# Kernel optimization log

Measured on AMD Instinct MI355X. Metric: run time of the kernel, lower is better.

## Reference

```python
import jax, jax.numpy as jnp
import numpy as np

B, Q, H, W, C = 2, 8192, 64, 64, 64
C9 = C * 9
EPS = 1e-6


def _mlp(x, params):
    # gelu MLP, no activation on last layer (matches repo mlp)
    for Wm, b in params[:-1]:
        x = jax.nn.gelu(x @ Wm + b)
    Wl, bl = params[-1]
    return x @ Wl + bl


def _make_coord(h, w):
    # pixel-center coords in (-1,1); channel 0 = row dim, channel 1 = col dim
    hs = -1.0 + (2.0 * jnp.arange(h, dtype=jnp.float32) + 1.0) / h
    ws = -1.0 + (2.0 * jnp.arange(w, dtype=jnp.float32) + 1.0) / w
    return jnp.stack(jnp.meshgrid(hs, ws, indexing='ij'), axis=0)  # (2,h,w)


def _nearest_gather(feat, coord):
    # F.grid_sample(mode='nearest', align_corners=False) on a (B,1,q,2) grid.
    # feat (B,C,H,W); coord (B,q,2) with [...,0] indexing H, [...,1] indexing W
    h, w = feat.shape[-2], feat.shape[-1]
    ih = jnp.clip(jnp.round((coord[..., 0] + 1.0) * h / 2.0 - 0.5), 0, h - 1).astype(jnp.int32)
    iw = jnp.clip(jnp.round((coord[..., 1] + 1.0) * w / 2.0 - 0.5), 0, w - 1).astype(jnp.int32)
    return jax.vmap(lambda f, a, b: f[:, a, b].T)(feat, ih, iw)  # (B,q,C)


def _unfold3(feat):
    # F.unfold(feat, 3, padding=1).view(B, C*9, H, W): channel-major, kernel row-major
    b, c, h, w = feat.shape
    p = jnp.pad(feat, ((0, 0), (0, 0), (1, 1), (1, 1)))
    patches = jnp.stack([p[:, :, i:i + h, j:j + w] for i in range(3) for j in range(3)], axis=2)
    return patches.reshape(b, c * 9, h, w)


def _forward(inp, coord, scale, enc_w, enc_b, iw0, ib0, iw1, ib1, iw2, ib2,
             sw0, sb0, sw1, sb1, ww0, wb0, ww1, wb1):
    # encoder (stand-in conv3x3, 3 -> C feature channels)
    feat = jax.lax.conv_general_dilated(inp, enc_w, (1, 1), 'SAME',
                                        dimension_numbers=('NCHW', 'OIHW', 'NCHW'))
    feat = feat + enc_b[None, :, None, None]
    feat = _unfold3(feat)  # (B, C*9, H, W)
    bsz, cf, h, w = feat.shape
    fcoord = jnp.broadcast_to(_make_coord(h, w)[None], (bsz, 2, h, w))
    dims = jnp.array([h, w], dtype=feat.dtype)

    tx = (h - 1) / (1.0 - scale[:, 0, 0])  # (B,)
    ty = (w - 1) / (1.0 - scale[:, 0, 1])
    rx, ry = 1.0 / tx, 1.0 / ty
    scale_tok = scale * dims  # (B,q,2)

    imnet_p = [(iw0, ib0), (iw1, ib1), (iw2, ib2)]
    score_p = [(sw0, sb0), (sw1, sb1)]
    weight_p = [(ww0, wb0), (ww1, wb1)]

    preds = []
    for vx in (-1, 1):
        for vy in (-1, 1):
            shift = jnp.stack([vx * rx + EPS, vy * ry + EPS], axis=-1)[:, None, :]  # (B,1,2)
            c = jnp.clip(coord + shift, -1.0 + 1e-6, 1.0 - 1e-6)
            value = _nearest_gather(feat, c)      # (B,q,C*9)
            coord_k = _nearest_gather(fcoord, c)  # (B,q,2)
            rel = (coord - coord_k) * dims        # (B,q,2)
            score = _mlp(rel, score_p)            # (B,q,1) -> broadcast over 3
            mlp_in = jnp.concatenate([rel, scale_tok], axis=-1)  # (B,q,4)
            wmat = _mlp(mlp_in, imnet_p).reshape(bsz, -1, cf, 3)  # (B,q,C*9,3)
            preds.append(jnp.einsum('bqc,bqck->bqk', value, wmat) + score)
    stacked = jnp.stack(preds, axis=-1)  # (B,q,3,4)
    return _mlp(stacked, weight_p)[..., 0]  # (B,q,3)


def setup_inputs() -> dict:
    key = jax.random.key(0)
    ks = jax.random.split(key, 16)
    f32 = jnp.float32

    def wi(k, shape, fan_in):
        return jax.random.normal(k, shape, f32) / np.float32(np.sqrt(fan_in))

    return {
        'inp': jax.random.normal(ks[0], (B, 3, H, W), f32),
        'coord': jax.random.uniform(ks[1], (B, Q, 2), f32, -1.0 + 1e-4, 1.0 - 1e-4),
        'scale': jax.random.uniform(ks[2], (B, Q, 2), f32, 0.01, 0.05),
        'enc_w': wi(ks[3], (C, 3, 3, 3), 27),
        'enc_b': jnp.zeros((C,), f32),
        'iw0': wi(ks[4], (4, 256), 4), 'ib0': jnp.zeros((256,), f32),
        'iw1': wi(ks[5], (256, 256), 256), 'ib1': jnp.zeros((256,), f32),
        'iw2': wi(ks[6], (256, C9 * 3), 256), 'ib2': jnp.zeros((C9 * 3,), f32),
        'sw0': wi(ks[7], (2, 256), 2), 'sb0': jnp.zeros((256,), f32),
        'sw1': wi(ks[8], (256, 1), 256), 'sb1': jnp.zeros((1,), f32),
        'ww0': wi(ks[9], (4, 256), 4), 'wb0': jnp.zeros((256,), f32),
        'ww1': wi(ks[10], (256, 1), 256), 'wb1': jnp.zeros((1,), f32),
    }


def reference(inp, coord, scale, enc_w, enc_b, iw0, ib0, iw1, ib1, iw2, ib2,
              sw0, sb0, sw1, sb1, ww0, wb0, ww1, wb1):
    return _forward(inp, coord, scale, enc_w, enc_b, iw0, ib0, iw1, ib1, iw2, ib2,
                    sw0, sb0, sw1, sb1, ww0, wb0, ww1, wb1)
```

## Files before the change

### kernel.cpp

```cpp
#include <hip/hip_runtime.h>

#define QN 8192
#define CCH 64
#define NROW 65536
#define MR 32
#define NBLK (NROW / MR)
#define H0S 264
#define UW 784
#define SVP 592

typedef _Float16 f16x8 __attribute__((ext_vector_type(8)));
typedef _Float16 f16x4 __attribute__((ext_vector_type(4)));
typedef _Float16 f16x2 __attribute__((ext_vector_type(2)));
typedef float f32x4 __attribute__((ext_vector_type(4)));

#if __has_builtin(__builtin_amdgcn_fdot2)
#define FDOT2(A, B, C) __builtin_amdgcn_fdot2((A), (B), (C), false)
#else
#define FDOT2(A, B, C) fmaf((float)(A)[1], (float)(B)[1], fmaf((float)(A)[0], (float)(B)[0], (C)))
#endif
#define DOT8(H, U, ACC) do {                                                                      \
    ACC = FDOT2(((f16x2){(H)[0], (H)[1]}), ((f16x2){(U)[0], (U)[1]}), ACC);                       \
    ACC = FDOT2(((f16x2){(H)[2], (H)[3]}), ((f16x2){(U)[2], (U)[3]}), ACC);                       \
    ACC = FDOT2(((f16x2){(H)[4], (H)[5]}), ((f16x2){(U)[4], (U)[5]}), ACC);                       \
    ACC = FDOT2(((f16x2){(H)[6], (H)[7]}), ((f16x2){(U)[6], (U)[7]}), ACC);                       \
} while (0)

__device__ __forceinline__ float gelu_f(float x) {
    float x2 = x * x;
    float tt = fmaf(0.044715f, x2, 1.0f);
    float e = __builtin_amdgcn_exp2f(2.3022081597f * x * tt);
    float r = __builtin_amdgcn_rcpf(1.0f + e);
    return x - x * r;
}

__global__ __launch_bounds__(256) void k_pre(const float* __restrict__ inp,
                                             const float* __restrict__ ew,
                                             const float* __restrict__ eb,
                                             const float* __restrict__ coord,
                                             const float* __restrict__ scale,
                                             const float* __restrict__ sw0,
                                             const float* __restrict__ sb0,
                                             const float* __restrict__ sw1,
                                             const float* __restrict__ sb1,
                                             const float* __restrict__ iw1,
                                             const float* __restrict__ iw2,
                                             const float* __restrict__ ib2,
                                             float* __restrict__ featpad,
                                             float4* __restrict__ mlp_in,
                                             int2* __restrict__ ihiw,
                                             float* __restrict__ scoreg,
                                             _Float16* __restrict__ w1tp,
                                             _Float16* __restrict__ w3tp) {
    const int bb = blockIdx.x;
    const int tt0 = threadIdx.x;
    if (bb < 2178) {
        __shared__ float s_ew[1728];
        for (int i = tt0; i < 1728; i += 256) s_ew[i] = ew[i];
        __syncthreads();
        int idx = bb * 256 + tt0;
        const int total = 2 * 66 * 66 * CCH;
        if (idx >= total) return;
        int o = idx & 63; int pix = idx >> 6;
        int xx = pix % 66; int t2 = pix / 66;
        int yy = t2 % 66;  int b = t2 / 66;
        int y = yy - 1, x = xx - 1;
        float acc = 0.0f;
        if (y >= 0 && y < 64 && x >= 0 && x < 64) {
            acc = eb[o];
            for (int i = 0; i < 3; ++i) {
                const float* ip = inp + ((b * 3 + i) * 64) * 64;
                const float* wp = s_ew + (o * 3 + i) * 9;
                #pragma unroll
                for (int ky = 0; ky < 3; ++ky) {
                    int sy = y + ky - 1;
                    if (sy < 0 || sy > 63) continue;
                    #pragma unroll
                    for (int kx = 0; kx < 3; ++kx) {
                        int sx = x + kx - 1;
                        if (sx < 0 || sx > 63) continue;
                        acc += ip[sy * 64 + sx] * wp[ky * 3 + kx];
                    }
                }
            }
        }
        featpad[idx] = acc;
    } else if (bb < 2434) {
        int row = (bb - 2178) * 256 + tt0;
        int v = row & 3;
        int bq = row >> 2;
        int b = bq >> 13;
        float c0 = coord[bq * 2 + 0], c1 = coord[bq * 2 + 1];
        float s0 = scale[bq * 2 + 0], s1 = scale[bq * 2 + 1];
        float s00 = scale[(b * QN) * 2 + 0];
        float s01 = scale[(b * QN) * 2 + 1];
        float rx = (1.0f - s00) / 63.0f;
        float ry = (1.0f - s01) / 63.0f;
        float vx = (v & 2) ? 1.0f : -1.0f;
        float vy = (v & 1) ? 1.0f : -1.0f;
        float cc0 = c0 + vx * rx + 1e-6f;
        float cc1 = c1 + vy * ry + 1e-6f;
        cc0 = fminf(fmaxf(cc0, -1.0f + 1e-6f), 1.0f - 1e-6f);
        cc1 = fminf(fmaxf(cc1, -1.0f + 1e-6f), 1.0f - 1e-6f);
        int ih = (int)rintf((cc0 + 1.0f) * 32.0f - 0.5f);
        int iw = (int)rintf((cc1 + 1.0f) * 32.0f - 0.5f);
        ih = min(max(ih, 0), 63);
        iw = min(max(iw, 0), 63);
        float ck0 = (2.0f * (float)ih + 1.0f) / 64.0f - 1.0f;
        float ck1 = (2.0f * (float)iw + 1.0f) / 64.0f - 1.0f;
        float rel0 = (c0 - ck0) * 64.0f;
        float rel1 = (c1 - ck1) * 64.0f;
        mlp_in[row] = make_float4(rel0, rel1, s0 * 64.0f, s1 * 64.0f);
        ihiw[row] = make_int2(ih, iw);
        float sc = sb1[0];
        #pragma unroll 4
        for (int t2 = 0; t2 < 256; ++t2) {
            float h = gelu_f(fmaf(rel0, sw0[t2], fmaf(rel1, sw0[256 + t2], sb0[t2])));
            sc = fmaf(h, sw1[t2], sc);
        }
        scoreg[row] = sc;
    } else {
        int idx = (bb - 2434) * 256 + tt0;
        if (idx < 451584) {
            int jj = idx & 7, ln = (idx >> 3) & 63;
            int tlkf = idx >> 9;
            int tl = tlkf / 18, kf = tlkf - tl * 18;
            int o = tl * 16 + (ln & 15);
            int v = kf * 32 + (ln >> 4) * 8 + jj;
            int tap = v >> 6, cch = v & 63;
            float val = 0.0f;
            if (o < 768) {
                int j = o & 255, k = o >> 8;
                val = iw2[j * 1728 + (cch * 9 + tap) * 3 + k];
            } else if (o < 771) {
                val = ib2[(cch * 9 + tap) * 3 + (o - 768)];
            }
            w3tp[idx] = (_Float16)val;
        } else {
            int i2 = idx - 451584;
            int j = i2 & 7, ln = (i2 >> 3) & 63, kf = (i2 >> 9) & 7, ct = i2 >> 12;
            int col = ct * 16 + (ln & 15);
            int kk = kf * 32 + (ln >> 4) * 8 + j;
            w1tp[i2] = (_Float16)iw1[kk * 256 + col];
        }
    }
}

__global__ __launch_bounds__(256) void k_u(const float* __restrict__ featpad,
                                           const _Float16* __restrict__ w3tp,
                                           _Float16* __restrict__ u) {
    __shared__ __align__(16) _Float16 s_val[32 * SVP];
    __shared__ int s_dtab[9];
    const int t = threadIdx.x;
    const int wave = t >> 6, lane = t & 63, quad = lane >> 4, l15 = lane & 15;
    if (t < 9) { int dy = t / 3; s_dtab[t] = (dy * 66 + (t - 3 * dy)) * 64; }
    {
        int p = t & 31, half = t >> 5;
        int slot = blockIdx.x * 32 + p;
        int b = slot >> 12, rem = slot & 4095, y = rem >> 6, x = rem & 63;
        int base = ((b * 66 + y) * 66 + x) * 64;
        __syncthreads();
        #pragma unroll
        for (int i = 0; i < 18; ++i) {
            int v0 = half * 72 + i * 4;
            int tap = v0 >> 6, cch = v0 & 63;
            float4 f = *(const float4*)(featpad + base + s_dtab[tap] + cch);
            f16x4 hv = {(_Float16)f.x, (_Float16)f.y, (_Float16)f.z, (_Float16)f.w};
            *(f16x4*)(s_val + p * SVP + v0) = hv;
        }
    }
    __syncthreads();

    const int t0 = (wave == 0) ? 0 : 1 + wave * 12;
    const int nt = (wave == 0) ? 13 : 12;
    #pragma unroll 1
    for (int tt = 0; tt < nt; ++tt) {
        int tl = t0 + tt;
        const _Float16* wp = w3tp + ((size_t)(tl * 18) * 64 + lane) * 8;
        f16x8 bbuf[18];
        #pragma unroll
        for (int kf = 0; kf < 18; ++kf) bbuf[kf] = *(const f16x8*)(wp + (size_t)kf * 512);
        f32x4 ac0 = {0.f, 0.f, 0.f, 0.f}, ac1 = {0.f, 0.f, 0.f, 0.f};
        #pragma unroll
        for (int kf = 0; kf < 18; ++kf) {
            f16x8 a0 = *(const f16x8*)(s_val + l15 * SVP + kf * 32 + quad * 8);
            f16x8 a1 = *(const f16x8*)(s_val + (16 + l15) * SVP + kf * 32 + quad * 8);
            ac0 = __builtin_amdgcn_mfma_f32_16x16x32_f16(a0, bbuf[kf], ac0, 0, 0, 0);
            ac1 = __builtin_amdgcn_mfma_f32_16x16x32_f16(a1, bbuf[kf], ac1, 0, 0, 0);
        }
        size_t pb = (size_t)(blockIdx.x * 32 + quad * 4) * UW + tl * 16 + l15;
        #pragma unroll
        for (int rg = 0; rg < 4; ++rg) u[pb + (size_t)rg * UW] = (_Float16)ac0[rg];
        pb += (size_t)16 * UW;
        #pragma unroll
        for (int rg = 0; rg < 4; ++rg) u[pb + (size_t)rg * UW] = (_Float16)ac1[rg];
    }
}

#define LDX1(B, CT) do { const _Float16* wp_ = w1tp + (size_t)((CT) * 8) * 512 + lane * 8;        \
    _Pragma("unroll") for (int kf_ = 0; kf_ < 4; ++kf_) B[kf_] = *(const f16x8*)(wp_ + kf_ * 512); } while (0)
#define LDY1(B, CT) do { const _Float16* wp_ = w1tp + (size_t)((CT) * 8 + 4) * 512 + lane * 8;    \
    _Pragma("unroll") for (int kf_ = 0; kf_ < 4; ++kf_) B[kf_] = *(const f16x8*)(wp_ + kf_ * 512); } while (0)
#define ZACCB(BV) do { _Pragma("unroll") for (int rt_ = 0; rt_ < 2; ++rt_)                        \
    acc[rt_] = (f32x4){(BV), (BV), (BV), (BV)}; } while (0)
#define MFMAH(B, OFS) do { _Pragma("unroll") for (int kf_ = 0; kf_ < 4; ++kf_)                    \
    { _Pragma("unroll") for (int rt_ = 0; rt_ < 2; ++rt_)                                         \
      acc[rt_] = __builtin_amdgcn_mfma_f32_16x16x32_f16(a[rt_][kf_ + (OFS)], B[kf_], acc[rt_], 0, 0, 0); } } while (0)
#define H1EPI(CT) do { int col_ = (CT) * 16 + l15;                                                \
    _Pragma("unroll") for (int rt_ = 0; rt_ < 2; ++rt_)                                           \
      { _Pragma("unroll") for (int rg_ = 0; rg_ < 4; ++rg_)                                       \
        s_h0[(rt_ * 16 + quad * 4 + rg_) * H0S + col_] = (_Float16)gelu_f(acc[rt_][rg_]); } } while (0)

__global__ __launch_bounds__(256, 3) void k_dot(const float4* __restrict__ mlp_in,
                                                const int2* __restrict__ ihiw,
                                                const float* __restrict__ iw0,
                                                const float* __restrict__ ib0,
                                                const _Float16* __restrict__ w1tp,
                                                const float* __restrict__ ib1,
                                                const _Float16* __restrict__ ubuf,
                                                const float* __restrict__ scoreg,
                                                const float* __restrict__ ww0,
                                                const float* __restrict__ wb0,
                                                const float* __restrict__ ww1,
                                                const float* __restrict__ wb1,
                                                float* __restrict__ out) {
    __shared__ __align__(16) _Float16 s_h0[MR * H0S];
    __shared__ float4 s_min[MR];
    __shared__ int    s_slot[MR];
    __shared__ float  s_pred[MR][3];
    __shared__ float  s_score[MR];
    __shared__ float  s_dred[MR][3][8];
    __shared__ float  s_wred[24][4];

    const int t = threadIdx.x;
    const int wave = t >> 6, lane = t & 63, quad = lane >> 4, l15 = lane & 15;
    const int rowbase = blockIdx.x * MR;

    if (t < MR) {
        int row = rowbase + t;
        s_min[t] = mlp_in[row];
        s_score[t] = scoreg[row];
        int b = row >> 15;
        int2 p = ihiw[row];
        s_slot[t] = (b << 12) + (p.x << 6) + p.y;
    }
    __syncthreads();

    {
        float w0 = iw0[t], w1 = iw0[256 + t], w2 = iw0[512 + t], w3 = iw0[768 + t];
        float bb = ib0[t];
        #pragma unroll 4
        for (int r = 0; r < MR; ++r) {
            float4 m = s_min[r];
            s_h0[r * H0S + t] =
                (_Float16)gelu_f(fmaf(m.x, w0, fmaf(m.y, w1, fmaf(m.z, w2, fmaf(m.w, w3, bb)))));
        }
    }
    __syncthreads();

    const int w4 = wave * 4;
    const float bibA = ib1[(w4 + 0) * 16 + l15];
    const float bibB = ib1[(w4 + 1) * 16 + l15];
    const float bibC = ib1[(w4 + 2) * 16 + l15];
    const float bibD = ib1[(w4 + 3) * 16 + l15];

    f16x8 bX0[4], bX1[4], bY0[4], bY1[4];
    f32x4 acc[2];

    LDX1(bX0, w4);
    LDY1(bY0, w4);
    LDX1(bX1, w4 + 1);

    f16x8 a[2][8];
    #pragma unroll
    for (int rt = 0; rt < 2; ++rt)
        #pragma unroll
        for (int kf = 0; kf < 8; ++kf)
            a[rt][kf] = *(const f16x8*)(s_h0 + (rt * 16 + l15) * H0S + kf * 32 + quad * 8);
    __syncthreads();

    LDY1(bY1, w4 + 1);
    ZACCB(bibA); MFMAH(bX0, 0);
    LDX1(bX0, w4 + 2);
    MFMAH(bY0, 4);
    H1EPI(w4);
    LDY1(bY0, w4 + 2);
    ZACCB(bibB); MFMAH(bX1, 0);
    LDX1(bX1, w4 + 3);
    MFMAH(bY1, 4);
    H1EPI(w4 + 1);
    LDY1(bY1, w4 + 3);
    ZACCB(bibC); MFMAH(bX0, 0);
    MFMAH(bY0, 4);
    H1EPI(w4 + 2);
    ZACCB(bibD); MFMAH(bX1, 0);
    MFMAH(bY1, 4);
    H1EPI(w4 + 3);
    __syncthreads();

    {
        int r = t >> 3, sub = t & 7;
        int j0 = sub * 32;
        const _Float16* hb = s_h0 + r * H0S + j0;
        const _Float16* ub = ubuf + (size_t)s_slot[r] * UW + j0;
        float a0 = 0.f, a1 = 0.f, a2 = 0.f;
        #pragma unroll
        for (int c = 0; c < 4; ++c) {
            f16x8 h8 = *(const f16x8*)(hb + c * 8);
            f16x8 u0 = *(const f16x8*)(ub + c * 8);
            f16x8 u1 = *(const f16x8*)(ub + 256 + c * 8);
            f16x8 u2 = *(const f16x8*)(ub + 512 + c * 8);
            DOT8(h8, u0, a0);
            DOT8(h8, u1, a1);
            DOT8(h8, u2, a2);
        }
        s_dred[r][0][sub] = a0;
        s_dred[r][1][sub] = a1;
        s_dred[r][2][sub] = a2;
    }
    __syncthreads();
    if (t < 96) {
        int r = t / 3, k = t - 3 * r;
        float s = (float)ubuf[(size_t)s_slot[r] * UW + 768 + k];
        #pragma unroll
        for (int q = 0; q < 8; ++q) s += s_dred[r][k][q];
        s_pred[r][k] = s;
    }
    __syncthreads();

    if (t < 96) {
        int o = t >> 2, sub = t & 3;
        int bql = o / 3, k = o - 3 * bql;
        float x0 = s_pred[bql * 4 + 0][k] + s_score[bql * 4 + 0];
        float x1 = s_pred[bql * 4 + 1][k] + s_score[bql * 4 + 1];
        float x2 = s_pred[bql * 4 + 2][k] + s_score[bql * 4 + 2];
        float x3 = s_pred[bql * 4 + 3][k] + s_score[bql * 4 + 3];
        float acc2 = 0.0f;
        int j0 = sub * 64;
        #pragma unroll 4
        for (int j = j0; j < j0 + 64; ++j) {
            float h = gelu_f(fmaf(x0, ww0[j], fmaf(x1, ww0[256 + j],
                          fmaf(x2, ww0[512 + j], fmaf(x3, ww0[768 + j], wb0[j])))));
            acc2 = fmaf(h, ww1[j], acc2);
        }
        s_wred[o][sub] = acc2;
    }
    __syncthreads();
    if (t < 24) {
        int bql = t / 3, k = t - 3 * bql;
        float r2 = s_wred[t][0] + s_wred[t][1] + s_wred[t][2] + s_wred[t][3] + wb1[0];
        out[(blockIdx.x * 8 + bql) * 3 + k] = r2;
    }
}

extern "C" void kernel_launch(void* const* d_in, const int* in_sizes, int n_in,
                              void* d_out, int out_size, void* d_ws, size_t ws_size,
                              hipStream_t stream) {
    const float* inp   = (const float*)d_in[0];
    const float* coord = (const float*)d_in[1];
    const float* scale = (const float*)d_in[2];
    const float* ew    = (const float*)d_in[3];
    const float* eb    = (const float*)d_in[4];
    const float* iw0   = (const float*)d_in[5];
    const float* ib0   = (const float*)d_in[6];
    const float* iw1   = (const float*)d_in[7];
    const float* ib1   = (const float*)d_in[8];
    const float* iw2   = (const float*)d_in[9];
    const float* ib2   = (const float*)d_in[10];
    const float* sw0   = (const float*)d_in[11];
    const float* sb0   = (const float*)d_in[12];
    const float* sw1   = (const float*)d_in[13];
    const float* sb1   = (const float*)d_in[14];
    const float* ww0   = (const float*)d_in[15];
    const float* wb0   = (const float*)d_in[16];
    const float* ww1   = (const float*)d_in[17];
    const float* wb1   = (const float*)d_in[18];
    float* out = (float*)d_out;

    char* ws = (char*)d_ws;
    float*     featpad = (float*)(ws + 0);
    float4*    mlp_in  = (float4*)(ws + 2230272);
    int2*      ihiw    = (int2*)(ws + 3278848);
    float*     scoreg  = (float*)(ws + 3803136);
    _Float16*  w1tp    = (_Float16*)(ws + 4065280);
    _Float16*  w3tp    = (_Float16*)(ws + 4196352);
    _Float16*  u       = (_Float16*)(ws + 5099520);

    k_pre<<<dim3(4454), dim3(256), 0, stream>>>(inp, ew, eb, coord, scale,
                                                sw0, sb0, sw1, sb1, iw1, iw2, ib2,
                                                featpad, mlp_in, ihiw, scoreg,
                                                w1tp, w3tp);
    k_u<<<dim3(256), dim3(256), 0, stream>>>(featpad, w3tp, u);
    k_dot<<<dim3(NBLK), dim3(256), 0, stream>>>(mlp_in, ihiw, iw0, ib0, w1tp, ib1,
                                                u, scoreg, ww0, wb0, ww1, wb1, out);
}
```

Before: 223.8 us.

## Split k_u tiles across 4x more blocks and coalesce weight-repack reads

The k_u launch grows from 256 to 1024 blocks. Each block now handles a strided subset of the 49 output tiles (one tile slot per wave) instead of every wave sweeping about 12 tiles, which raises occupancy on the many-CU GPU. In exchange, each 32-row patch staging into shared memory is repeated 4 times. Separately, the iw2/iw1 repack in k_pre now reads the source weights linearly and scatters the writes, so the global reads coalesce instead of being strided.

```diff
diff --git a/kernel.cpp b/kernel.cpp
--- a/kernel.cpp
+++ b/kernel.cpp
@@ -121,42 +121,50 @@
         scoreg[row] = sc;
     } else {
         int idx = (bb - 2434) * 256 + tt0;
-        if (idx < 451584) {
-            int jj = idx & 7, ln = (idx >> 3) & 63;
-            int tlkf = idx >> 9;
-            int tl = tlkf / 18, kf = tlkf - tl * 18;
-            int o = tl * 16 + (ln & 15);
-            int v = kf * 32 + (ln >> 4) * 8 + jj;
+        if (idx < 442368) {
+            float val = iw2[idx];
+            int j = idx / 1728, n = idx - j * 1728;
+            int k = n % 3, m = n / 3;
+            int tap = m % 9, cch = m / 9;
+            int o = k * 256 + j;
+            int v = tap * 64 + cch;
+            int tl = o >> 4, kf = v >> 5;
+            int ln = (((v & 31) >> 3) << 4) | (o & 15);
+            int jj = v & 7;
+            w3tp[((tl * 18 + kf) * 64 + ln) * 8 + jj] = (_Float16)val;
+        } else if (idx < 451584) {
+            int e = idx - 442368;
+            int jj = e & 7, ln = (e >> 3) & 63, kf = e >> 9;
+            int o16 = ln & 15;
+            int v = kf * 32 + ((ln >> 4) << 3) + jj;
             int tap = v >> 6, cch = v & 63;
-            float val = 0.0f;
-            if (o < 768) {
-                int j = o & 255, k = o >> 8;
-                val = iw2[j * 1728 + (cch * 9 + tap) * 3 + k];
-            } else if (o < 771) {
-                val = ib2[(cch * 9 + tap) * 3 + (o - 768)];
-            }
-            w3tp[idx] = (_Float16)val;
+            float val = (o16 < 3) ? ib2[(cch * 9 + tap) * 3 + o16] : 0.0f;
+            w3tp[((48 * 18 + kf) * 64 + ln) * 8 + jj] = (_Float16)val;
         } else {
-            int i2 = idx - 451584;
-            int j = i2 & 7, ln = (i2 >> 3) & 63, kf = (i2 >> 9) & 7, ct = i2 >> 12;
-            int col = ct * 16 + (ln & 15);
-            int kk = kf * 32 + (ln >> 4) * 8 + j;
-            w1tp[i2] = (_Float16)iw1[kk * 256 + col];
+            int f2 = idx - 451584;
+            float val = iw1[f2];
+            int kk = f2 >> 8, col = f2 & 255;
+            int ct = col >> 4, kf = kk >> 5;
+            int ln = (((kk & 31) >> 3) << 4) | (col & 15);
+            int jj = kk & 7;
+            w1tp[((ct * 8 + kf) * 64 + ln) * 8 + jj] = (_Float16)val;
         }
     }
 }
 
-__global__ __launch_bounds__(256) void k_u(const float* __restrict__ featpad,
-                                           const _Float16* __restrict__ w3tp,
-                                           _Float16* __restrict__ u) {
+__global__ __launch_bounds__(256, 4) void k_u(const float* __restrict__ featpad,
+                                              const _Float16* __restrict__ w3tp,
+                                              _Float16* __restrict__ u) {
     __shared__ __align__(16) _Float16 s_val[32 * SVP];
     __shared__ int s_dtab[9];
     const int t = threadIdx.x;
     const int wave = t >> 6, lane = t & 63, quad = lane >> 4, l15 = lane & 15;
+    const int pg = blockIdx.x & 255;
+    const int slotid = ((blockIdx.x >> 8) << 2) | wave;
     if (t < 9) { int dy = t / 3; s_dtab[t] = (dy * 66 + (t - 3 * dy)) * 64; }
     {
         int p = t & 31, half = t >> 5;
-        int slot = blockIdx.x * 32 + p;
+        int slot = pg * 32 + p;
         int b = slot >> 12, rem = slot & 4095, y = rem >> 6, x = rem & 63;
         int base = ((b * 66 + y) * 66 + x) * 64;
         __syncthreads();
@@ -171,11 +179,8 @@
     }
     __syncthreads();
 
-    const int t0 = (wave == 0) ? 0 : 1 + wave * 12;
-    const int nt = (wave == 0) ? 13 : 12;
     #pragma unroll 1
-    for (int tt = 0; tt < nt; ++tt) {
-        int tl = t0 + tt;
+    for (int tl = slotid; tl < 49; tl += 16) {
         const _Float16* wp = w3tp + ((size_t)(tl * 18) * 64 + lane) * 8;
         f16x8 bbuf[18];
         #pragma unroll
@@ -188,7 +193,7 @@
             ac0 = __builtin_amdgcn_mfma_f32_16x16x32_f16(a0, bbuf[kf], ac0, 0, 0, 0);
             ac1 = __builtin_amdgcn_mfma_f32_16x16x32_f16(a1, bbuf[kf], ac1, 0, 0, 0);
         }
-        size_t pb = (size_t)(blockIdx.x * 32 + quad * 4) * UW + tl * 16 + l15;
+        size_t pb = (size_t)(pg * 32 + quad * 4) * UW + tl * 16 + l15;
         #pragma unroll
         for (int rg = 0; rg < 4; ++rg) u[pb + (size_t)rg * UW] = (_Float16)ac0[rg];
         pb += (size_t)16 * UW;
@@ -390,7 +395,7 @@
                                                 sw0, sb0, sw1, sb1, iw1, iw2, ib2,
                                                 featpad, mlp_in, ihiw, scoreg,
                                                 w1tp, w3tp);
-    k_u<<<dim3(256), dim3(256), 0, stream>>>(featpad, w3tp, u);
+    k_u<<<dim3(1024), dim3(256), 0, stream>>>(featpad, w3tp, u);
     k_dot<<<dim3(NBLK), dim3(256), 0, stream>>>(mlp_in, ihiw, iw0, ib0, w1tp, ib1,
                                                 u, scoreg, ww0, wb0, ww1, wb1, out);
 }
```

After: 240.3 us. 1.07x slower.
